# Performance work log

Hardware: AMD Instinct MI355X
Metric: run time of the kernel (lower is better)

Reference implementation:

```python
import jax, jax.numpy as jnp
import numpy as np

N_NODES = 10000
N_EDGES = 640000
F_NODE = 128   # n_node_features
F_EDGE = 128   # hiddens (edge_attr width)


def setup_inputs() -> dict:
    key = jax.random.key(0)
    k1, k2, k3, k4 = jax.random.split(key, 4)
    x = jax.random.normal(k1, (N_NODES, F_NODE), dtype=jnp.float32)
    edge_index = jax.random.randint(k2, (2, N_EDGES), 0, N_NODES, dtype=jnp.int64)
    edge_attr = jax.random.normal(k3, (N_EDGES, F_EDGE), dtype=jnp.float32)
    u = jax.random.normal(k4, (1, 16), dtype=jnp.float32)
    batch = jnp.zeros((N_NODES,), dtype=jnp.int64)
    return {"x": x, "edge_index": edge_index, "edge_attr": edge_attr, "u": u, "batch": batch}


def reference(x, edge_index, edge_attr, u, batch):
    # row: destination (scatter target), col: source (gather index)
    row, col = edge_index[0], edge_index[1]
    n = x.shape[0]
    # [E, F_NODE + F_EDGE]: gather source node feats, concat edge feats
    msg = jnp.concatenate([x[col], edge_attr], axis=1)
    # scatter_mean over destination nodes (count clamped to 1, matching torch_scatter)
    summed = jax.ops.segment_sum(msg, row, num_segments=n)
    counts = jax.ops.segment_sum(jnp.ones((row.shape[0],), x.dtype), row, num_segments=n)
    mean = summed / jnp.maximum(counts, 1.0)[:, None]
    # [N, 2*F_NODE + F_EDGE]
    return jnp.concatenate([x, mean], axis=1)
```

## Files before the change

kernel.cpp:

```cpp
#include <hip/hip_runtime.h>
#include <hip/hip_bf16.h>

#define F_NODE 128
#define F_EDGE 128
#define MSG_W  (F_NODE + F_EDGE)
#define OUT_W  (F_NODE + MSG_W)

__global__ void count_kernel(const int* __restrict__ row, int* __restrict__ counts, int E) {
    int e = blockIdx.x * blockDim.x + threadIdx.x;
    if (e < E) atomicAdd(&counts[row[e]], 1);
}

__global__ __launch_bounds__(1024) void scan_kernel(const int* __restrict__ counts,
                                                    int* __restrict__ offsets,
                                                    int* __restrict__ cursor, int n) {
    __shared__ int s[1024];
    __shared__ int carry_s;
    const int t = threadIdx.x;
    if (t == 0) carry_s = 0;
    __syncthreads();
    for (int base = 0; base < n; base += 1024) {
        int v = (base + t < n) ? counts[base + t] : 0;
        s[t] = v;
        __syncthreads();
        for (int off = 1; off < 1024; off <<= 1) {
            int add = (t >= off) ? s[t - off] : 0;
            __syncthreads();
            s[t] += add;
            __syncthreads();
        }
        int incl  = s[t];
        int carry = carry_s;
        __syncthreads();
        if (t == 1023) carry_s = carry + incl;
        if (base + t < n) {
            int excl = carry + incl - v;
            offsets[base + t] = excl;
            cursor[base + t]  = excl;
        }
        __syncthreads();
    }
    if (t == 0) offsets[n] = carry_s;
}

__global__ void scatter_kernel(const int* __restrict__ row, int* __restrict__ cursor,
                               int* __restrict__ edge_sorted, int E) {
    int e = blockIdx.x * blockDim.x + threadIdx.x;
    if (e < E) {
        int pos = atomicAdd(&cursor[row[e]], 1);
        edge_sorted[pos] = e;
    }
}

#define TILE 64
__global__ __launch_bounds__(256) void aggregate_kernel(
    const float* __restrict__ x, const int* __restrict__ col_idx,
    const float* __restrict__ edge_attr, const int* __restrict__ offsets,
    const int* __restrict__ edge_sorted, float* __restrict__ out, int n_nodes) {

    const int node = blockIdx.x;
    if (node >= n_nodes) return;
    const int t = threadIdx.x;

    const int start = offsets[node];
    const int end   = offsets[node + 1];

    __shared__ int s_e[TILE];
    __shared__ int s_c[TILE];

    float sum = 0.0f;
    for (int base = start; base < end; base += TILE) {
        const int m = min(TILE, end - base);
        if (t < m) {
            int e   = edge_sorted[base + t];
            s_e[t]  = e;
            s_c[t]  = col_idx[e];
        }
        __syncthreads();
        if (t < F_NODE) {
            for (int i = 0; i < m; ++i)
                sum += x[(size_t)s_c[i] * F_NODE + t];
        } else {
            const int tt = t - F_NODE;
            for (int i = 0; i < m; ++i)
                sum += edge_attr[(size_t)s_e[i] * F_EDGE + tt];
        }
        __syncthreads();
    }

    const float cnt  = (float)(end - start);
    const float mean = sum * (1.0f / fmaxf(cnt, 1.0f));

    float* orow = out + (size_t)node * OUT_W;
    orow[F_NODE + t] = mean;
    if (t < F_NODE) orow[t] = x[(size_t)node * F_NODE + t];
}

extern "C" void kernel_launch(void* const* d_in, const int* in_sizes, int n_in,
                              void* d_out, int out_size, void* d_ws, size_t ws_size,
                              hipStream_t stream) {
    const float* x          = (const float*)d_in[0];
    const int*   edge_index = (const int*)d_in[1];
    const float* edge_attr  = (const float*)d_in[2];

    const int n_nodes = in_sizes[0] / F_NODE;
    const int E       = in_sizes[1] / 2;
    const int* row = edge_index;
    const int* col = edge_index + E;

    int* counts      = (int*)d_ws;
    int* offsets     = counts + n_nodes;
    int* cursor      = offsets + n_nodes + 1;
    int* edge_sorted = cursor + n_nodes;

    float* out = (float*)d_out;

    hipMemsetAsync(counts, 0, (size_t)n_nodes * sizeof(int), stream);

    const int TB = 256;
    count_kernel<<<(E + TB - 1) / TB, TB, 0, stream>>>(row, counts, E);
    scan_kernel<<<1, 1024, 0, stream>>>(counts, offsets, cursor, n_nodes);
    scatter_kernel<<<(E + TB - 1) / TB, TB, 0, stream>>>(row, cursor, edge_sorted, E);
    aggregate_kernel<<<n_nodes, 256, 0, stream>>>(x, col, edge_attr, offsets,
                                                  edge_sorted, out, n_nodes);
}
```

Before: 560.9 us.

## Use wave-per-node float4 aggregation with packed edge/col pairs and shuffle scan

The aggregation moves from one 256-thread block per node to one 64-lane wave per node. Each lane loads a float4, half the lanes read x and half read edge_attr, and edge and column indices are broadcast with shuffles, so shared memory and block barriers are gone. The scatter step now writes (edge, col) pairs so aggregation avoids the dependent col_idx load. The single-block scan becomes a chunked serial-plus-wave-shuffle scan with far fewer barriers. Each lane holds more in-flight work, and the per-lane chunked scan reads memory uncoalesced.

```diff
diff --git a/kernel.cpp b/kernel.cpp
--- a/kernel.cpp
+++ b/kernel.cpp
@@ -3,97 +3,99 @@
 
 #define F_NODE 128
 #define F_EDGE 128
-#define MSG_W  (F_NODE + F_EDGE)
-#define OUT_W  (F_NODE + MSG_W)
+#define OUT_W  384
 
 __global__ void count_kernel(const int* __restrict__ row, int* __restrict__ counts, int E) {
     int e = blockIdx.x * blockDim.x + threadIdx.x;
     if (e < E) atomicAdd(&counts[row[e]], 1);
 }
 
-__global__ __launch_bounds__(1024) void scan_kernel(const int* __restrict__ counts,
-                                                    int* __restrict__ offsets,
-                                                    int* __restrict__ cursor, int n) {
-    __shared__ int s[1024];
-    __shared__ int carry_s;
+__global__ __launch_bounds__(256) void scan_kernel(const int* __restrict__ counts,
+                                                   int* __restrict__ offsets,
+                                                   int* __restrict__ cursor, int n) {
     const int t = threadIdx.x;
-    if (t == 0) carry_s = 0;
+    const int chunk = (n + 255) / 256;
+    const int lo = t * chunk;
+    const int hi = min(lo + chunk, n);
+
+    int local = 0;
+    for (int i = lo; i < hi; ++i) local += counts[i];
+
+    const int lane = t & 63, wv = t >> 6;
+    int incl = local;
+    for (int d = 1; d < 64; d <<= 1) {
+        int v = __shfl_up(incl, d);
+        if (lane >= d) incl += v;
+    }
+    __shared__ int wsum[4];
+    if (lane == 63) wsum[wv] = incl;
     __syncthreads();
-    for (int base = 0; base < n; base += 1024) {
-        int v = (base + t < n) ? counts[base + t] : 0;
-        s[t] = v;
-        __syncthreads();
-        for (int off = 1; off < 1024; off <<= 1) {
-            int add = (t >= off) ? s[t - off] : 0;
-            __syncthreads();
-            s[t] += add;
-            __syncthreads();
-        }
-        int incl  = s[t];
-        int carry = carry_s;
-        __syncthreads();
-        if (t == 1023) carry_s = carry + incl;
-        if (base + t < n) {
-            int excl = carry + incl - v;
-            offsets[base + t] = excl;
-            cursor[base + t]  = excl;
-        }
-        __syncthreads();
+    int wpre = 0;
+    for (int w = 0; w < wv; ++w) wpre += wsum[w];
+    int run = wpre + incl - local;
+
+    for (int i = lo; i < hi; ++i) {
+        offsets[i] = run;
+        cursor[i]  = run;
+        run += counts[i];
     }
-    if (t == 0) offsets[n] = carry_s;
+    if (t == 255) offsets[n] = wpre + incl;
 }
 
-__global__ void scatter_kernel(const int* __restrict__ row, int* __restrict__ cursor,
-                               int* __restrict__ edge_sorted, int E) {
+__global__ void scatter_kernel(const int* __restrict__ row, const int* __restrict__ col,
+                               int* __restrict__ cursor, int2* __restrict__ pairs, int E) {
     int e = blockIdx.x * blockDim.x + threadIdx.x;
     if (e < E) {
-        int pos = atomicAdd(&cursor[row[e]], 1);
-        edge_sorted[pos] = e;
+        int r = row[e];
+        int c = col[e];
+        int pos = atomicAdd(&cursor[r], 1);
+        pairs[pos] = make_int2(e, c);
     }
 }
 
-#define TILE 64
 __global__ __launch_bounds__(256) void aggregate_kernel(
-    const float* __restrict__ x, const int* __restrict__ col_idx,
-    const float* __restrict__ edge_attr, const int* __restrict__ offsets,
-    const int* __restrict__ edge_sorted, float* __restrict__ out, int n_nodes) {
+    const float* __restrict__ x, const float* __restrict__ edge_attr,
+    const int* __restrict__ offsets, const int2* __restrict__ pairs,
+    float* __restrict__ out, int n_nodes) {
 
-    const int node = blockIdx.x;
+    const int wave = threadIdx.x >> 6;
+    const int lane = threadIdx.x & 63;
+    const int node = blockIdx.x * 4 + wave;
     if (node >= n_nodes) return;
-    const int t = threadIdx.x;
 
     const int start = offsets[node];
     const int end   = offsets[node + 1];
+    const int cnt   = end - start;
 
-    __shared__ int s_e[TILE];
-    __shared__ int s_c[TILE];
+    const bool is_x = lane < 32;
+    const int  sub4 = (is_x ? lane : (lane - 32)) * 4;
 
-    float sum = 0.0f;
-    for (int base = start; base < end; base += TILE) {
-        const int m = min(TILE, end - base);
-        if (t < m) {
-            int e   = edge_sorted[base + t];
-            s_e[t]  = e;
-            s_c[t]  = col_idx[e];
+    float4 sum = make_float4(0.f, 0.f, 0.f, 0.f);
+
+    for (int base = start; base < end; base += 64) {
+        const int m = min(64, end - base);
+        int idx = base + lane;
+        if (idx >= end) idx = end - 1;
+        const int2 pr = pairs[idx];
+        for (int i = 0; i < m; ++i) {
+            const int e = __shfl(pr.x, i);
+            const int c = __shfl(pr.y, i);
+            const float* px = x         + (size_t)c * F_NODE;
+            const float* pe = edge_attr + (size_t)e * F_EDGE;
+            const float* p  = (is_x ? px : pe) + sub4;
+            const float4 v = *(const float4*)p;
+            sum.x += v.x; sum.y += v.y; sum.z += v.z; sum.w += v.w;
         }
-        __syncthreads();
-        if (t < F_NODE) {
-            for (int i = 0; i < m; ++i)
-                sum += x[(size_t)s_c[i] * F_NODE + t];
-        } else {
-            const int tt = t - F_NODE;
-            for (int i = 0; i < m; ++i)
-                sum += edge_attr[(size_t)s_e[i] * F_EDGE + tt];
-        }
-        __syncthreads();
     }
 
-    const float cnt  = (float)(end - start);
-    const float mean = sum * (1.0f / fmaxf(cnt, 1.0f));
+    const float inv = 1.0f / fmaxf((float)cnt, 1.0f);
+    float* orow = out + (size_t)node * OUT_W;
 
-    float* orow = out + (size_t)node * OUT_W;
-    orow[F_NODE + t] = mean;
-    if (t < F_NODE) orow[t] = x[(size_t)node * F_NODE + t];
+    float4 mean = make_float4(sum.x * inv, sum.y * inv, sum.z * inv, sum.w * inv);
+    *(float4*)(orow + F_NODE + lane * 4) = mean;
+
+    const float* xr = x + (size_t)node * F_NODE;
+    *(float2*)(orow + lane * 2) = *(const float2*)(xr + lane * 2);
 }
 
 extern "C" void kernel_launch(void* const* d_in, const int* in_sizes, int n_in,
@@ -108,10 +110,10 @@
     const int* row = edge_index;
     const int* col = edge_index + E;
 
-    int* counts      = (int*)d_ws;
-    int* offsets     = counts + n_nodes;
-    int* cursor      = offsets + n_nodes + 1;
-    int* edge_sorted = cursor + n_nodes;
+    int2* pairs   = (int2*)d_ws;
+    int*  counts  = (int*)(pairs + E);
+    int*  offsets = counts + n_nodes;
+    int*  cursor  = offsets + n_nodes + 1;
 
     float* out = (float*)d_out;
 
@@ -119,8 +121,8 @@
 
     const int TB = 256;
     count_kernel<<<(E + TB - 1) / TB, TB, 0, stream>>>(row, counts, E);
-    scan_kernel<<<1, 1024, 0, stream>>>(counts, offsets, cursor, n_nodes);
-    scatter_kernel<<<(E + TB - 1) / TB, TB, 0, stream>>>(row, cursor, edge_sorted, E);
-    aggregate_kernel<<<n_nodes, 256, 0, stream>>>(x, col, edge_attr, offsets,
-                                                  edge_sorted, out, n_nodes);
+    scan_kernel<<<1, 256, 0, stream>>>(counts, offsets, cursor, n_nodes);
+    scatter_kernel<<<(E + TB - 1) / TB, TB, 0, stream>>>(row, col, cursor, pairs, E);
+    aggregate_kernel<<<(n_nodes + 3) / 4, 256, 0, stream>>>(x, edge_attr, offsets,
+                                                            pairs, out, n_nodes);
 }
```

After: 584.9 us. 1.04x slower.
